# Kernel optimization log

Hardware: AMD Instinct MI355X
Metric: run time of the kernel (lower is better)

Reference implementation:

```python
import jax, jax.numpy as jnp
import numpy as np

B, C, H, W = 32, 512, 64, 64
K = 512  # num_embeddings == embedding_dim == C (required by the original view())
COMMIT = 0.25


def setup_inputs() -> dict:
    key = jax.random.key(0)
    k1, k2 = jax.random.split(key)
    x = jax.random.normal(k1, (B, C, H, W), dtype=jnp.float32)
    # nn.Embedding weight init: uniform(-1/K, 1/K)
    embed = jax.random.uniform(k2, (K, C), dtype=jnp.float32, minval=-1.0 / K, maxval=1.0 / K)
    return {"x": x, "embed": embed}


def reference(x, embed):
    # BCHW -> BHWC
    inputs = jnp.transpose(x, (0, 2, 3, 1))  # [B,H,W,C]
    flat = inputs.reshape(-1, C)              # [N,C], N = B*H*W
    d = (jnp.sum(flat * flat, axis=1, keepdims=True)
         + jnp.sum(embed * embed, axis=1)
         - 2.0 * flat @ embed.T)              # [N,K]
    idx = jnp.argmin(d, axis=1)               # [N]
    # one-hot @ embed  ==  gather
    quantized = embed[idx].reshape(inputs.shape)  # [B,H,W,C]

    e_latent = jnp.mean((jax.lax.stop_gradient(quantized) - inputs) ** 2)
    q_latent = jnp.mean((quantized - jax.lax.stop_gradient(inputs)) ** 2)
    loss = q_latent + COMMIT * e_latent

    # straight-through estimator
    quant_st = inputs + jax.lax.stop_gradient(quantized - inputs)

    # perplexity (as in source: mean over batch of #unique codes used)
    idx_b = idx.reshape(B, -1)                # [B, H*W]

    def n_unique(i):
        cnt = jnp.zeros((K,), jnp.int32).at[i].add(1)
        return jnp.sum(cnt > 0)

    perplexity = jnp.mean(jax.vmap(n_unique)(idx_b).astype(jnp.float32))

    return loss, jnp.transpose(quant_st, (0, 3, 1, 2)), perplexity, idx_b
```

## Files before the change

kernel.cpp:

```cpp
#include <hip/hip_runtime.h>
#include <stdint.h>

#define B_ 32
#define C_ 512
#define HW_ 4096
#define N_ 131072
#define K_ 512
#define QELEMS 67108864
#define MARGIN 1e-3f
#define RFCAP 131072

typedef __attribute__((ext_vector_type(8)))  short bf16x8;
typedef __attribute__((ext_vector_type(16))) float f32x16;

__device__ __forceinline__ ushort f2bf(float f) {
  uint u = __float_as_uint(f);
  return (ushort)((u + 0x7FFFu + ((u >> 16) & 1u)) >> 16);
}

__device__ __forceinline__ float np_pw512(const float* a) {
  float P[4];
#pragma unroll
  for (int m = 0; m < 4; ++m) {
    const float* q = a + m * 128;
    float rv[16];
#pragma unroll
    for (int l = 0; l < 16; ++l) {
      float v0 = q[l],      v1 = q[16 + l],  v2 = q[32 + l],  v3 = q[48 + l];
      float v4 = q[64 + l], v5 = q[80 + l],  v6 = q[96 + l],  v7 = q[112 + l];
      rv[l] = ((v0 + v1) + (v2 + v3)) + ((v4 + v5) + (v6 + v7));
    }
    float u[8], w[4];
#pragma unroll
    for (int l = 0; l < 8; ++l) u[l] = rv[8 + l] + rv[l];
#pragma unroll
    for (int l = 0; l < 4; ++l) w[l] = u[4 + l] + u[l];
    P[m] = (w[0] + w[2]) + (w[1] + w[3]);
  }
  return (P[0] + P[1]) + (P[2] + P[3]);
}

__device__ __forceinline__ float np_pw512_sq(const float* a) {
  float P[4];
#pragma unroll
  for (int m = 0; m < 4; ++m) {
    const float* q = a + m * 128;
    float rv[16];
#pragma unroll
    for (int l = 0; l < 16; ++l) {
      float v0 = __fmul_rn(q[l], q[l]);
      float v1 = __fmul_rn(q[16 + l], q[16 + l]);
      float v2 = __fmul_rn(q[32 + l], q[32 + l]);
      float v3 = __fmul_rn(q[48 + l], q[48 + l]);
      float v4 = __fmul_rn(q[64 + l], q[64 + l]);
      float v5 = __fmul_rn(q[80 + l], q[80 + l]);
      float v6 = __fmul_rn(q[96 + l], q[96 + l]);
      float v7 = __fmul_rn(q[112 + l], q[112 + l]);
      rv[l] = ((v0 + v1) + (v2 + v3)) + ((v4 + v5) + (v6 + v7));
    }
    float u[8], w[4];
#pragma unroll
    for (int l = 0; l < 8; ++l) u[l] = rv[8 + l] + rv[l];
#pragma unroll
    for (int l = 0; l < 4; ++l) w[l] = u[4 + l] + u[l];
    P[m] = (w[0] + w[2]) + (w[1] + w[3]);
  }
  return (P[0] + P[1]) + (P[2] + P[3]);
}

__global__ __launch_bounds__(256) void k_prep(const float* __restrict__ embed,
    float* __restrict__ senp, float* __restrict__ eT, int* __restrict__ rcnt)
{
  __shared__ float sqa[C_];
  int k = blockIdx.x;
  for (int c = threadIdx.x; c < C_; c += 256) {
    float e = embed[k * C_ + c];
    eT[c * K_ + k] = e;
    sqa[c] = __fmul_rn(e, e);
  }
  __syncthreads();
  if (threadIdx.x == 0) {
    senp[k] = np_pw512(sqa);
    if (blockIdx.x == 0) *rcnt = 0;
  }
}

__global__ __launch_bounds__(256) void k_epack(const float* __restrict__ embed,
    ushort* __restrict__ efrag)
{
  const int cb = blockIdx.x;
  const int t = threadIdx.x;
  const int lane = t & 63, ksq = t >> 6;
  const int l31 = lane & 31, lhi = lane >> 5;
  const float* ep = embed + ((size_t)(cb * 32 + l31) << 9) + lhi * 8;
#pragma unroll
  for (int i = 0; i < 8; ++i) {
    int ks = ksq * 8 + i;
    float4 v0 = *(const float4*)(ep + ks * 16);
    float4 v1 = *(const float4*)(ep + ks * 16 + 4);
    uint u0 = (uint)f2bf(v0.x) | ((uint)f2bf(v0.y) << 16);
    uint u1 = (uint)f2bf(v0.z) | ((uint)f2bf(v0.w) << 16);
    uint u2 = (uint)f2bf(v1.x) | ((uint)f2bf(v1.y) << 16);
    uint u3 = (uint)f2bf(v1.z) | ((uint)f2bf(v1.w) << 16);
    ushort* op = efrag + (((size_t)(cb * 32 + ks)) * 64 + lane) * 8;
    *(uint4*)op = make_uint4(u0, u1, u2, u3);
  }
}

__global__ __launch_bounds__(256) void k_xsplit(const float* __restrict__ x,
    ushort* __restrict__ xfrag, float* __restrict__ xT)
{
  __shared__ float tile[64][66];
  const int bid = blockIdx.x;
  const int ht = bid & 63, ct = (bid >> 6) & 7, b = bid >> 9;
  const int t = threadIdx.x;
  const int r = t & 63, cq = t >> 6;
  const float* xp = x + (((size_t)(b * C_ + ct * 64)) << 12) + ht * 64 + r;
#pragma unroll
  for (int i = 0; i < 16; ++i) {
    int c = cq * 16 + i;
    tile[r][c] = xp[(size_t)c << 12];
  }
  __syncthreads();
  const int lane = t & 63, ksl = t >> 6;
  const int l31 = lane & 31, lhi = lane >> 5;
  const int ks = ct * 4 + ksl;
  const int cc = ksl * 16 + lhi * 8;
#pragma unroll
  for (int rbl = 0; rbl < 2; ++rbl) {
    int rr = rbl * 32 + l31;
    uint u[4];
#pragma unroll
    for (int j = 0; j < 4; ++j) {
      float f0 = tile[rr][cc + 2 * j];
      float f1 = tile[rr][cc + 2 * j + 1];
      u[j] = (uint)f2bf(f0) | ((uint)f2bf(f1) << 16);
    }
    size_t rb = (size_t)b * 128 + ht * 2 + rbl;
    ushort* op = xfrag + ((rb * 32 + ks) * 64 + lane) * 8;
    *(uint4*)op = make_uint4(u[0], u[1], u[2], u[3]);
  }
  if (xT) {
    const int r2 = t >> 2, cs2 = (t & 3) << 4;
    float* op = xT + ((size_t)(b * HW_ + ht * 64 + r2) << 9) + ct * 64 + cs2;
#pragma unroll
    for (int j = 0; j < 4; ++j) {
      float4 v;
      v.x = tile[r2][cs2 + 4 * j + 0];
      v.y = tile[r2][cs2 + 4 * j + 1];
      v.z = tile[r2][cs2 + 4 * j + 2];
      v.w = tile[r2][cs2 + 4 * j + 3];
      *(float4*)(op + 4 * j) = v;
    }
  }
}

__global__ __launch_bounds__(512) void k_argmin(const ushort* __restrict__ xfrag,
    const ushort* __restrict__ efrag, const float* __restrict__ senp,
    int* __restrict__ idx_out, int* __restrict__ rcnt, int* __restrict__ rrows)
{
  __shared__ float ses[K_];
  __shared__ float mbL[64][4], msL[64][4];
  __shared__ int   miL[64][4];
  const int t = threadIdx.x;
  const int lane = t & 63, wid = t >> 6;
  const int wc = wid & 3, wr = wid >> 2;
  const int l31 = lane & 31, lhi = lane >> 5;
  const int b = blockIdx.x >> 6;
  const int rowt = blockIdx.x & 63;

  for (int i = t; i < K_; i += 512) ses[i] = senp[i];
  __syncthreads();

  const size_t rb = (size_t)b * 128 + rowt * 2 + wr;
  const bf16x8* xq  = (const bf16x8*)xfrag + rb * 32 * 64 + lane;
  const bf16x8* eq0 = (const bf16x8*)efrag + (size_t)(wc * 4 + 0) * 32 * 64 + lane;
  const bf16x8* eq1 = (const bf16x8*)efrag + (size_t)(wc * 4 + 1) * 32 * 64 + lane;
  const bf16x8* eq2 = (const bf16x8*)efrag + (size_t)(wc * 4 + 2) * 32 * 64 + lane;
  const bf16x8* eq3 = (const bf16x8*)efrag + (size_t)(wc * 4 + 3) * 32 * 64 + lane;

  f32x16 a0 = {0,0,0,0,0,0,0,0,0,0,0,0,0,0,0,0};
  f32x16 a1 = a0, a2 = a0, a3 = a0;
#pragma unroll 8
  for (int ks = 0; ks < 32; ++ks) {
    bf16x8 xf = xq[ks * 64];
    a0 = __builtin_amdgcn_mfma_f32_32x32x16_bf16(eq0[ks * 64], xf, a0, 0, 0, 0);
    a1 = __builtin_amdgcn_mfma_f32_32x32x16_bf16(eq1[ks * 64], xf, a1, 0, 0, 0);
    a2 = __builtin_amdgcn_mfma_f32_32x32x16_bf16(eq2[ks * 64], xf, a2, 0, 0, 0);
    a3 = __builtin_amdgcn_mfma_f32_32x32x16_bf16(eq3[ks * 64], xf, a3, 0, 0, 0);
  }

  float best = 1e30f, second = 1e30f; int bidx = 0;
#pragma unroll
  for (int r = 0; r < 16; ++r) {
    int crow = (r & 3) + 8 * (r >> 2) + 4 * lhi;
    float v; int code;
    code = wc * 128 + 0  + crow; v = ses[code] - 2.0f * a0[r];
    if (v < best || (v == best && code < bidx)) { second = best; best = v; bidx = code; }
    else if (v < second) second = v;
    code = wc * 128 + 32 + crow; v = ses[code] - 2.0f * a1[r];
    if (v < best || (v == best && code < bidx)) { second = best; best = v; bidx = code; }
    else if (v < second) second = v;
    code = wc * 128 + 64 + crow; v = ses[code] - 2.0f * a2[r];
    if (v < best || (v == best && code < bidx)) { second = best; best = v; bidx = code; }
    else if (v < second) second = v;
    code = wc * 128 + 96 + crow; v = ses[code] - 2.0f * a3[r];
    if (v < best || (v == best && code < bidx)) { second = best; best = v; bidx = code; }
    else if (v < second) second = v;
  }
  {
    float ob = __shfl_xor(best, 32, 64);
    float os = __shfl_xor(second, 32, 64);
    int   oi = __shfl_xor(bidx, 32, 64);
    float ns = fminf(fmaxf(best, ob), fminf(second, os));
    if (ob < best || (ob == best && oi < bidx)) { best = ob; bidx = oi; }
    second = ns;
  }
  if (lane < 32) {
    int rr = wr * 32 + l31;
    mbL[rr][wc] = best; msL[rr][wc] = second; miL[rr][wc] = bidx;
  }
  __syncthreads();
  if (t < 64) {
    float Bv = 1e30f, Sv = 1e30f; int Iv = 0;
#pragma unroll
    for (int q = 0; q < 4; ++q) {
      float b1 = mbL[t][q], s1 = msL[t][q]; int i1 = miL[t][q];
      if (b1 < Bv || (b1 == Bv && i1 < Iv)) { Sv = fminf(Bv, s1); Bv = b1; Iv = i1; }
      else Sv = fminf(Sv, b1);
    }
    int n = b * HW_ + rowt * 64 + t;
    idx_out[n] = Iv;
    if (Sv - Bv < MARGIN) {
      int p = atomicAdd(rcnt, 1);
      if (p < RFCAP) rrows[p] = n;
    }
  }
}

__global__ __launch_bounds__(512) void k_refine(const float* __restrict__ x,
    const float* __restrict__ xT, const float* __restrict__ eT,
    const float* __restrict__ senp,
    const int* __restrict__ rcnt, const int* __restrict__ rrows,
    int* __restrict__ idx_out)
{
  __shared__ float xls[8][520];
  __shared__ float SxSh[8];
  __shared__ int   nrow[8];
  __shared__ float wval[8][8];
  __shared__ int   widx[8][8];
  const int t = threadIdx.x;
  const int lane = t & 63, w = t >> 6;
  int cnt = *rcnt; if (cnt > RFCAP) cnt = RFCAP;
  for (int base = blockIdx.x * 8; base < cnt; base += gridDim.x * 8) {
    __syncthreads();
    if (t < 8) {
      int i = base + t;
      nrow[t] = rrows[i < cnt ? i : base];
    }
    __syncthreads();
    if (xT) {
#pragma unroll
      for (int rr = 0; rr < 8; ++rr)
        xls[rr][t] = xT[((size_t)nrow[rr] << 9) + t];
    } else {
#pragma unroll
      for (int rr = 0; rr < 8; ++rr) {
        int n = nrow[rr];
        int b = n >> 12, hw = n & 4095;
        xls[rr][t] = x[(((size_t)(b * C_ + t)) << 12) + hw];
      }
    }
    __syncthreads();
    if (t < 8) SxSh[t] = np_pw512_sq(&xls[t][0]);
    __syncthreads();
    const float* ep = eT + t;
    float a1[8], a2[8];
#pragma unroll
    for (int rr = 0; rr < 8; ++rr) { a1[rr] = 0.f; a2[rr] = 0.f; }
    for (int c4 = 0; c4 < 384; c4 += 4) {
      float e0 = ep[(size_t)(c4 + 0) << 9];
      float e1 = ep[(size_t)(c4 + 1) << 9];
      float e2 = ep[(size_t)(c4 + 2) << 9];
      float e3 = ep[(size_t)(c4 + 3) << 9];
#pragma unroll
      for (int rr = 0; rr < 8; ++rr) {
        float4 xv = *(const float4*)&xls[rr][c4];
        a1[rr] = fmaf(xv.x, e0, a1[rr]);
        a1[rr] = fmaf(xv.y, e1, a1[rr]);
        a1[rr] = fmaf(xv.z, e2, a1[rr]);
        a1[rr] = fmaf(xv.w, e3, a1[rr]);
      }
    }
    for (int c4 = 384; c4 < 512; c4 += 4) {
      float e0 = ep[(size_t)(c4 + 0) << 9];
      float e1 = ep[(size_t)(c4 + 1) << 9];
      float e2 = ep[(size_t)(c4 + 2) << 9];
      float e3 = ep[(size_t)(c4 + 3) << 9];
#pragma unroll
      for (int rr = 0; rr < 8; ++rr) {
        float4 xv = *(const float4*)&xls[rr][c4];
        a2[rr] = fmaf(xv.x, e0, a2[rr]);
        a2[rr] = fmaf(xv.y, e1, a2[rr]);
        a2[rr] = fmaf(xv.z, e2, a2[rr]);
        a2[rr] = fmaf(xv.w, e3, a2[rr]);
      }
    }
    float se = senp[t];
    float bv[8]; int bi[8];
#pragma unroll
    for (int rr = 0; rr < 8; ++rr) {
      float M = a1[rr] + a2[rr];
      bv[rr] = (SxSh[rr] + se) - 2.0f * M;
      bi[rr] = t;
    }
#pragma unroll
    for (int off = 1; off < 64; off <<= 1) {
#pragma unroll
      for (int rr = 0; rr < 8; ++rr) {
        float ov = __shfl_xor(bv[rr], off, 64);
        int   oi = __shfl_xor(bi[rr], off, 64);
        if (ov < bv[rr] || (ov == bv[rr] && oi < bi[rr])) { bv[rr] = ov; bi[rr] = oi; }
      }
    }
    if (lane == 0) {
#pragma unroll
      for (int rr = 0; rr < 8; ++rr) { wval[w][rr] = bv[rr]; widx[w][rr] = bi[rr]; }
    }
    __syncthreads();
    if (t < 8) {
      float Bv = wval[0][t]; int Iv = widx[0][t];
#pragma unroll
      for (int q = 1; q < 8; ++q) {
        float ov = wval[q][t]; int oi = widx[q][t];
        if (ov < Bv || (ov == Bv && oi < Iv)) { Bv = ov; Iv = oi; }
      }
      if (base + t < cnt) idx_out[nrow[t]] = Iv;
    }
  }
}

__global__ __launch_bounds__(256) void k_gather(const float* __restrict__ x,
    const float* __restrict__ embed, const int* __restrict__ idx,
    float* __restrict__ out_q, double* __restrict__ loss_part)
{
  __shared__ float ecol[32][512];
  const int bid = blockIdx.x;
  const int hch = bid & 1, cch = (bid >> 1) & 15, b = bid >> 5;
  const int c0 = cch * 32, hw0 = hch * 2048;
  const int t = threadIdx.x;
  for (int i = t; i < 512 * 32; i += 256) {
    int c = i & 31, k = i >> 5;
    ecol[c][(k + c0 + c) & 511] = embed[((size_t)k << 9) + c0 + c];
  }
  __syncthreads();
  int kreg[8];
#pragma unroll
  for (int j = 0; j < 8; ++j)
    kreg[j] = idx[(b << 12) + hw0 + t + 256 * j];
  double s = 0.0;
  for (int c = 0; c < 32; ++c) {
    const float* xrow = x + (((size_t)(b * C_ + c0 + c)) << 12) + hw0;
    float* orow = out_q + (((size_t)(b * C_ + c0 + c)) << 12) + hw0;
#pragma unroll
    for (int j = 0; j < 8; ++j) {
      float q  = ecol[c][(kreg[j] + c0 + c) & 511];
      float xv = xrow[t + 256 * j];
      orow[t + 256 * j] = q;
      double d = (double)q - (double)xv;
      s += d * d;
    }
  }
  for (int off = 32; off > 0; off >>= 1) s += __shfl_down(s, off, 64);
  __shared__ double wsum[4];
  if ((t & 63) == 0) wsum[t >> 6] = s;
  __syncthreads();
  if (t == 0)
    loss_part[bid] = (wsum[0] + wsum[1]) + (wsum[2] + wsum[3]);
}

__global__ __launch_bounds__(256) void k_pplx(const int* __restrict__ idx,
    float* __restrict__ out_idxf, int* __restrict__ counts)
{
  __shared__ int flags[K_];
  __shared__ int red[256];
  int b = blockIdx.x;
  for (int i = threadIdx.x; i < K_; i += 256) flags[i] = 0;
  __syncthreads();
  for (int hw = threadIdx.x; hw < HW_; hw += 256) {
    int k = idx[(b << 12) + hw];
    flags[k] = 1;
    out_idxf[(b << 12) + hw] = (float)k;
  }
  __syncthreads();
  int c = 0;
  for (int i = threadIdx.x; i < K_; i += 256) c += flags[i];
  red[threadIdx.x] = c;
  __syncthreads();
  for (int st = 128; st > 0; st >>= 1) {
    if (threadIdx.x < st) red[threadIdx.x] += red[threadIdx.x + st];
    __syncthreads();
  }
  if (threadIdx.x == 0) counts[b] = red[0];
}

__global__ __launch_bounds__(256) void k_final(const double* __restrict__ loss_part,
    const int* __restrict__ counts, float* __restrict__ out_loss,
    float* __restrict__ out_pplx)
{
  __shared__ double sred[256];
  double s = 0.0;
  for (int i = threadIdx.x; i < 1024; i += 256) s += loss_part[i];
  sred[threadIdx.x] = s;
  __syncthreads();
  for (int st = 128; st > 0; st >>= 1) {
    if (threadIdx.x < st) sred[threadIdx.x] += sred[threadIdx.x + st];
    __syncthreads();
  }
  if (threadIdx.x == 0) {
    *out_loss = (float)(1.25 * sred[0] / (double)QELEMS);
    int c = 0;
    for (int i = 0; i < B_; ++i) c += counts[i];
    *out_pplx = (float)c / (float)B_;
  }
}

extern "C" void kernel_launch(void* const* d_in, const int* in_sizes, int n_in,
                              void* d_out, int out_size, void* d_ws, size_t ws_size,
                              hipStream_t stream)
{
  const float* x     = (const float*)d_in[0];
  const float* embed = (const float*)d_in[1];
  float* out      = (float*)d_out;
  float* out_loss = out;
  float* out_q    = out + 1;
  float* out_pplx = out + 1 + QELEMS;
  float* out_idxf = out + 2 + QELEMS;

  char* ws = (char*)d_ws;
  int*    w_idx = (int*)ws;
  double* w_lp  = (double*)(ws + 524288);
  int*    w_cnt = (int*)(ws + 524288 + 16384);
  size_t pers = 524288 + 16384 + 128;

  const size_t SZ_XFR  = 134217728;
  const size_t SZ_EFR  = 524288;
  const size_t SZ_SENP = 2048;
  const size_t SZ_RCNT = 256;
  const size_t SZ_RROW = (size_t)RFCAP * 4;
  const size_t SZ_ET   = (size_t)K_ * C_ * 4;
  const size_t SZ_XT   = (size_t)N_ * C_ * 4;
  const size_t VOL_SMALL = SZ_XFR + SZ_EFR + SZ_SENP + SZ_RCNT + SZ_RROW + SZ_ET;
  const size_t VOL_BIG   = VOL_SMALL + SZ_XT;

  char* vbase;
  float* w_xT = nullptr;
  if (ws_size >= pers + VOL_BIG + 4096) {
    vbase = ws + ((pers + 255) & ~(size_t)255);
    w_xT  = (float*)(vbase + VOL_SMALL);
  } else if (ws_size >= pers + VOL_SMALL + 4096) {
    vbase = ws + ((pers + 255) & ~(size_t)255);
  } else {
    uintptr_t a = ((uintptr_t)(out_q + QELEMS) - VOL_SMALL) & ~(uintptr_t)255;
    vbase = (char*)a;
  }
  ushort* w_xfr  = (ushort*)vbase;
  ushort* w_efr  = (ushort*)(vbase + SZ_XFR);
  float*  w_senp = (float*)(vbase + SZ_XFR + SZ_EFR);
  int*    w_rcnt = (int*)(vbase + SZ_XFR + SZ_EFR + SZ_SENP);
  int*    w_rrows= (int*)(vbase + SZ_XFR + SZ_EFR + SZ_SENP + SZ_RCNT);
  float*  w_eT   = (float*)(vbase + SZ_XFR + SZ_EFR + SZ_SENP + SZ_RCNT + SZ_RROW);

  k_prep  <<<dim3(512),   dim3(256), 0, stream>>>(embed, w_senp, w_eT, w_rcnt);
  k_epack <<<dim3(16),    dim3(256), 0, stream>>>(embed, w_efr);
  k_xsplit<<<dim3(16384), dim3(256), 0, stream>>>(x, w_xfr, w_xT);
  k_argmin<<<dim3(2048),  dim3(512), 0, stream>>>(w_xfr, w_efr, w_senp, w_idx, w_rcnt, w_rrows);
  k_refine<<<dim3(2048),  dim3(512), 0, stream>>>(x, w_xT, w_eT, w_senp, w_rcnt, w_rrows, w_idx);
  k_gather<<<dim3(1024),  dim3(256), 0, stream>>>(x, embed, w_idx, out_q, w_lp);
  k_pplx  <<<dim3(32),    dim3(256), 0, stream>>>(w_idx, out_idxf, w_cnt);
  k_final <<<dim3(1),     dim3(256), 0, stream>>>(w_lp, w_cnt, out_loss, out_pplx);
}
```

Baseline: 585.3 us.

## Refine ambiguous rows over a short candidate list instead of all codes

For rows whose best and second-best bf16 distances are within the margin, the argmin kernel now records every code whose approximate distance falls within a wider threshold of the best, up to 16 per row. A new lightweight refine kernel recomputes exact fp32 distances only for those candidates, with one wave per row. Rows whose candidate list overflows go to a fallback list handled by the old full refine kernel. This removes most of the full 512-code fp32 recompute for near-tie rows. It adds atomics, extra workspace and an extra launch, and it relies on the bf16 error staying below the candidate threshold.

```diff
diff --git a/kernel.cpp b/kernel.cpp
--- a/kernel.cpp
+++ b/kernel.cpp
@@ -8,6 +8,8 @@
 #define K_ 512
 #define QELEMS 67108864
 #define MARGIN 1e-3f
+#define CAND   2.5e-3f
+#define MAXC   16
 #define RFCAP 131072
 
 typedef __attribute__((ext_vector_type(8)))  short bf16x8;
@@ -69,10 +71,12 @@
 }
 
 __global__ __launch_bounds__(256) void k_prep(const float* __restrict__ embed,
-    float* __restrict__ senp, float* __restrict__ eT, int* __restrict__ rcnt)
+    float* __restrict__ senp, float* __restrict__ eT, int* __restrict__ rcnt,
+    int* __restrict__ ocnt, int* __restrict__ candCnt)
 {
   __shared__ float sqa[C_];
   int k = blockIdx.x;
+  candCnt[blockIdx.x * 256 + threadIdx.x] = 0;
   for (int c = threadIdx.x; c < C_; c += 256) {
     float e = embed[k * C_ + c];
     eT[c * K_ + k] = e;
@@ -81,7 +85,7 @@
   __syncthreads();
   if (threadIdx.x == 0) {
     senp[k] = np_pw512(sqa);
-    if (blockIdx.x == 0) *rcnt = 0;
+    if (blockIdx.x == 0) { *rcnt = 0; *ocnt = 0; }
   }
 }
 
@@ -157,11 +161,14 @@
 
 __global__ __launch_bounds__(512) void k_argmin(const ushort* __restrict__ xfrag,
     const ushort* __restrict__ efrag, const float* __restrict__ senp,
-    int* __restrict__ idx_out, int* __restrict__ rcnt, int* __restrict__ rrows)
+    int* __restrict__ idx_out, int* __restrict__ rcnt, int* __restrict__ rrows,
+    int* __restrict__ candCnt, int* __restrict__ cand)
 {
   __shared__ float ses[K_];
   __shared__ float mbL[64][4], msL[64][4];
   __shared__ int   miL[64][4];
+  __shared__ float rowBest[64];
+  __shared__ int   rowFlag[64];
   const int t = threadIdx.x;
   const int lane = t & 63, wid = t >> 6;
   const int wc = wid & 3, wr = wid >> 2;
@@ -231,14 +238,105 @@
     }
     int n = b * HW_ + rowt * 64 + t;
     idx_out[n] = Iv;
-    if (Sv - Bv < MARGIN) {
+    rowBest[t] = Bv;
+    int fl = (Sv - Bv < MARGIN) ? 1 : 0;
+    rowFlag[t] = fl;
+    if (fl) {
       int p = atomicAdd(rcnt, 1);
       if (p < RFCAP) rrows[p] = n;
     }
   }
-}
-
-__global__ __launch_bounds__(512) void k_refine(const float* __restrict__ x,
+  __syncthreads();
+  {
+    const int rr = wr * 32 + l31;
+    if (rowFlag[rr]) {
+      const float thr = rowBest[rr] + CAND;
+      const int n = b * HW_ + rowt * 64 + rr;
+#pragma unroll
+      for (int r = 0; r < 16; ++r) {
+        int crow = (r & 3) + 8 * (r >> 2) + 4 * lhi;
+        float v; int code;
+        code = wc * 128 + 0  + crow; v = ses[code] - 2.0f * a0[r];
+        if (v <= thr) { int p = atomicAdd(&candCnt[n], 1); if (p < MAXC) cand[(size_t)n * MAXC + p] = code; }
+        code = wc * 128 + 32 + crow; v = ses[code] - 2.0f * a1[r];
+        if (v <= thr) { int p = atomicAdd(&candCnt[n], 1); if (p < MAXC) cand[(size_t)n * MAXC + p] = code; }
+        code = wc * 128 + 64 + crow; v = ses[code] - 2.0f * a2[r];
+        if (v <= thr) { int p = atomicAdd(&candCnt[n], 1); if (p < MAXC) cand[(size_t)n * MAXC + p] = code; }
+        code = wc * 128 + 96 + crow; v = ses[code] - 2.0f * a3[r];
+        if (v <= thr) { int p = atomicAdd(&candCnt[n], 1); if (p < MAXC) cand[(size_t)n * MAXC + p] = code; }
+      }
+    }
+  }
+}
+
+__global__ __launch_bounds__(256) void k_refine(const float* __restrict__ x,
+    const float* __restrict__ xT, const float* __restrict__ embed,
+    const float* __restrict__ senp,
+    const int* __restrict__ rcnt, const int* __restrict__ rrows,
+    const int* __restrict__ candCnt, const int* __restrict__ cand,
+    int* __restrict__ ocnt, int* __restrict__ olist,
+    int* __restrict__ idx_out)
+{
+  __shared__ float xls[4][516];
+  __shared__ float SxSh[4];
+  __shared__ int   nrow[4];
+  const int t = threadIdx.x;
+  const int lane = t & 63, w = t >> 6;
+  int cnt = *rcnt; if (cnt > RFCAP) cnt = RFCAP;
+  for (int base = blockIdx.x * 4; base < cnt; base += gridDim.x * 4) {
+    __syncthreads();
+    if (t < 4) {
+      int i = base + t;
+      nrow[t] = rrows[i < cnt ? i : base];
+    }
+    __syncthreads();
+    if (xT) {
+      for (int i = t; i < 4 * C_; i += 256) {
+        int s = i >> 9, c = i & 511;
+        xls[s][c] = xT[((size_t)nrow[s] << 9) + c];
+      }
+    } else {
+      for (int i = t; i < 4 * C_; i += 256) {
+        int s = i >> 9, c = i & 511;
+        int n = nrow[s];
+        int b = n >> 12, hw = n & 4095;
+        xls[s][c] = x[(((size_t)(b * C_ + c)) << 12) + hw];
+      }
+    }
+    __syncthreads();
+    if (t < 4) SxSh[t] = np_pw512_sq(&xls[t][0]);
+    __syncthreads();
+    const int n = nrow[w];
+    const int cc = candCnt[n];
+    float d = 1e30f; int code = 0x7fffffff;
+    if (cc <= MAXC) {
+      if (lane < cc) {
+        code = cand[(size_t)n * MAXC + lane];
+        const float* e = embed + (size_t)code * C_;
+        const float* xr = &xls[w][0];
+        float s1 = 0.f, s2 = 0.f;
+        for (int c = 0; c < 384; ++c)  s1 = fmaf(xr[c], e[c], s1);
+        for (int c = 384; c < 512; ++c) s2 = fmaf(xr[c], e[c], s2);
+        float M = s1 + s2;
+        d = (SxSh[w] + senp[code]) - 2.0f * M;
+      }
+#pragma unroll
+      for (int off = 1; off < 16; off <<= 1) {
+        float ov = __shfl_xor(d, off, 64);
+        int   oc = __shfl_xor(code, off, 64);
+        if (ov < d || (ov == d && oc < code)) { d = ov; code = oc; }
+      }
+      if (lane == 0 && base + w < cnt) idx_out[n] = code;
+    } else {
+      if (lane == 0 && base + w < cnt) {
+        int p = atomicAdd(ocnt, 1);
+        if (p < RFCAP) olist[p] = n;
+      }
+    }
+  }
+}
+
+__global__ __launch_bounds__(512) void k_refine_full(const float* __restrict__ x,
     const float* __restrict__ xT, const float* __restrict__ eT,
     const float* __restrict__ senp,
     const int* __restrict__ rcnt, const int* __restrict__ rrows,
@@ -448,9 +546,13 @@
   const size_t SZ_SENP = 2048;
   const size_t SZ_RCNT = 256;
   const size_t SZ_RROW = (size_t)RFCAP * 4;
+  const size_t SZ_OLST = (size_t)RFCAP * 4;
   const size_t SZ_ET   = (size_t)K_ * C_ * 4;
+  const size_t SZ_CCNT = (size_t)N_ * 4;
+  const size_t SZ_CAND = (size_t)N_ * MAXC * 4;
   const size_t SZ_XT   = (size_t)N_ * C_ * 4;
-  const size_t VOL_SMALL = SZ_XFR + SZ_EFR + SZ_SENP + SZ_RCNT + SZ_RROW + SZ_ET;
+  const size_t VOL_SMALL = SZ_XFR + SZ_EFR + SZ_SENP + SZ_RCNT + SZ_RROW +
+                           SZ_OLST + SZ_ET + SZ_CCNT + SZ_CAND;
   const size_t VOL_BIG   = VOL_SMALL + SZ_XT;
 
   char* vbase;
@@ -464,18 +566,24 @@
     uintptr_t a = ((uintptr_t)(out_q + QELEMS) - VOL_SMALL) & ~(uintptr_t)255;
     vbase = (char*)a;
   }
-  ushort* w_xfr  = (ushort*)vbase;
-  ushort* w_efr  = (ushort*)(vbase + SZ_XFR);
-  float*  w_senp = (float*)(vbase + SZ_XFR + SZ_EFR);
-  int*    w_rcnt = (int*)(vbase + SZ_XFR + SZ_EFR + SZ_SENP);
-  int*    w_rrows= (int*)(vbase + SZ_XFR + SZ_EFR + SZ_SENP + SZ_RCNT);
-  float*  w_eT   = (float*)(vbase + SZ_XFR + SZ_EFR + SZ_SENP + SZ_RCNT + SZ_RROW);
-
-  k_prep  <<<dim3(512),   dim3(256), 0, stream>>>(embed, w_senp, w_eT, w_rcnt);
+  char* p = vbase;
+  ushort* w_xfr  = (ushort*)p;            p += SZ_XFR;
+  ushort* w_efr  = (ushort*)p;            p += SZ_EFR;
+  float*  w_senp = (float*)p;             p += SZ_SENP;
+  int*    w_rcnt = (int*)p;
+  int*    w_ocnt = (int*)(p + 128);       p += SZ_RCNT;
+  int*    w_rrows= (int*)p;               p += SZ_RROW;
+  int*    w_olst = (int*)p;               p += SZ_OLST;
+  float*  w_eT   = (float*)p;             p += SZ_ET;
+  int*    w_ccnt = (int*)p;               p += SZ_CCNT;
+  int*    w_cand = (int*)p;               p += SZ_CAND;
+
+  k_prep  <<<dim3(512),   dim3(256), 0, stream>>>(embed, w_senp, w_eT, w_rcnt, w_ocnt, w_ccnt);
   k_epack <<<dim3(16),    dim3(256), 0, stream>>>(embed, w_efr);
   k_xsplit<<<dim3(16384), dim3(256), 0, stream>>>(x, w_xfr, w_xT);
-  k_argmin<<<dim3(2048),  dim3(512), 0, stream>>>(w_xfr, w_efr, w_senp, w_idx, w_rcnt, w_rrows);
-  k_refine<<<dim3(2048),  dim3(512), 0, stream>>>(x, w_xT, w_eT, w_senp, w_rcnt, w_rrows, w_idx);
+  k_argmin<<<dim3(2048),  dim3(512), 0, stream>>>(w_xfr, w_efr, w_senp, w_idx, w_rcnt, w_rrows, w_ccnt, w_cand);
+  k_refine<<<dim3(2048),  dim3(256), 0, stream>>>(x, w_xT, embed, w_senp, w_rcnt, w_rrows, w_ccnt, w_cand, w_ocnt, w_olst, w_idx);
+  k_refine_full<<<dim3(256), dim3(512), 0, stream>>>(x, w_xT, w_eT, w_senp, w_ocnt, w_olst, w_idx);
   k_gather<<<dim3(1024),  dim3(256), 0, stream>>>(x, embed, w_idx, out_q, w_lp);
   k_pplx  <<<dim3(32),    dim3(256), 0, stream>>>(w_idx, out_idxf, w_cnt);
   k_final <<<dim3(1),     dim3(256), 0, stream>>>(w_lp, w_cnt, out_loss, out_pplx);
```

After: 573.8 us. -2.0%, faster.
